# Optimization experiments

Hardware: AMD Instinct MI355X
Metric: run time of the kernel (lower is better)

Reference implementation:

```python
import jax, jax.numpy as jnp
import numpy as np

N, F, H, L = 1536, 32, 64, 3  # num_nodes, num_features, hidden, num_layers
NEG_SLOPE = 0.01
BN_EPS = 1e-5


def _lrelu(x):
    return jnp.where(x >= 0, x, NEG_SLOPE * x)


def _gin_layer(x, src, tgt, eps, w1, b1, w2, b2, g, be):
    # scatter-add aggregation: out[tgt] += x[src] (source_to_target flow)
    agg = jax.ops.segment_sum(x[src], tgt, num_segments=N)
    h = (1.0 + eps) * x + agg
    h = jax.nn.relu(h @ w1 + b1)
    h = jax.nn.relu(h @ w2 + b2)
    # BatchNorm1d, training-mode (batch statistics, biased variance)
    mean = jnp.mean(h, axis=0)
    var = jnp.mean((h - mean) ** 2, axis=0)
    return (h - mean) * jax.lax.rsqrt(var + BN_EPS) * g + be


def setup_inputs() -> dict:
    key = jax.random.key(0)
    ks = iter(jax.random.split(key, 40))

    def rn(shape, scale=0.05):
        return jax.random.normal(next(ks), shape, dtype=jnp.float32) * scale

    inp = {
        "x": rn((N, F), 1.0),
        "node_features": rn((N, F), 1.0),
        # conv1: F -> H
        "c1_eps": jnp.zeros((), jnp.float32),
        "c1_w1": rn((F, H)), "c1_b1": jnp.zeros((H,), jnp.float32),
        "c1_w2": rn((H, H)), "c1_b2": jnp.zeros((H,), jnp.float32),
        "c1_g": jnp.ones((H,), jnp.float32), "c1_be": jnp.zeros((H,), jnp.float32),
        # L-1 additional GIN convs: H -> H (stacked)
        "cv_eps": jnp.zeros((L - 1,), jnp.float32),
        "cv_w1": rn((L - 1, H, H)), "cv_b1": jnp.zeros((L - 1, H), jnp.float32),
        "cv_w2": rn((L - 1, H, H)), "cv_b2": jnp.zeros((L - 1, H), jnp.float32),
        "cv_g": jnp.ones((L - 1, H), jnp.float32), "cv_be": jnp.zeros((L - 1, H), jnp.float32),
        # projection head
        "lin1_w": rn((H, H)), "lin1_b": jnp.zeros((H,), jnp.float32),
        "lin2_w": rn((H, F)), "lin2_b": jnp.zeros((F,), jnp.float32),
        # edge predictor: 2F -> H -> H -> H -> 1
        "ep_w1": rn((2 * F, H)), "ep_b1": jnp.zeros((H,), jnp.float32),
        "ep_w2": rn((H, H)), "ep_b2": jnp.zeros((H,), jnp.float32),
        "ep_w3": rn((H, H)), "ep_b3": jnp.zeros((H,), jnp.float32),
        "ep_w4": rn((H, 1)), "ep_b4": jnp.zeros((1,), jnp.float32),
    }
    return inp


def reference(x, node_features, c1_eps, c1_w1, c1_b1, c1_w2, c1_b2, c1_g, c1_be,
              cv_eps, cv_w1, cv_b1, cv_w2, cv_b2, cv_g, cv_be,
              lin1_w, lin1_b, lin2_w, lin2_b,
              ep_w1, ep_b1, ep_w2, ep_b2, ep_w3, ep_b3, ep_w4, ep_b4):
    # complete-graph upper-triangular edge list (matches torch.combinations order)
    src, tgt = jnp.triu_indices(N, k=1)
    h = node_features  # forward ignores input x
    xinit = h
    h = _lrelu(_gin_layer(h, src, tgt, c1_eps, c1_w1, c1_b1, c1_w2, c1_b2, c1_g, c1_be))
    for i in range(L - 1):
        h = _lrelu(_gin_layer(h, src, tgt, cv_eps[i], cv_w1[i], cv_b1[i],
                              cv_w2[i], cv_b2[i], cv_g[i], cv_be[i]))
    h = _lrelu(h @ lin1_w + lin1_b)
    h = _lrelu(h @ lin2_w + lin2_b)
    h = h + xinit  # [N, F]

    # edge predictor: gather -> MLP -> sigmoid over E edges
    ef = jnp.concatenate([h[src], h[tgt]], axis=-1)  # [E, 2F]
    e = jax.nn.relu(ef @ ep_w1 + ep_b1)
    e = jax.nn.relu(e @ ep_w2 + ep_b2)
    e = jax.nn.relu(e @ ep_w3 + ep_b3)
    e = jax.nn.sigmoid(e @ ep_w4 + ep_b4)[:, 0]  # [E]

    probs = jnp.zeros((N, N), dtype=h.dtype)
    probs = probs.at[src, tgt].set(e).at[tgt, src].set(e)
    return probs
```

## Files before the change

### kernel.cpp

```cpp
#include <hip/hip_runtime.h>
#include <math.h>

#define NN 1536
#define FF 32
#define HH 64
#define EE (NN*(NN-1)/2)
#define EBLK 2493
#define BN_EPS 1e-5f
#define SLOPE 0.01f

typedef _Float16 v8h  __attribute__((ext_vector_type(8)));
typedef __fp16   v2hf __attribute__((ext_vector_type(2)));
typedef float    f32x4 __attribute__((ext_vector_type(4)));

union V8H { v8h v; v2hf h2[4]; float4 f4; };

__device__ __forceinline__ float lrelu_f(float v){ return v >= 0.f ? v : SLOPE*v; }
__device__ __forceinline__ f32x4 lrelu4(f32x4 v) {
  f32x4 r;
#pragma unroll
  for (int j = 0; j < 4; ++j) r[j] = v[j] >= 0.f ? v[j] : SLOPE*v[j];
  return r;
}

template<int DIN, bool FIRST>
__global__ __launch_bounds__(512) void k_gin(
    const float* __restrict__ zin,
    const float* __restrict__ gg, const float* __restrict__ be,
    const float* __restrict__ eps_p,
    const float* __restrict__ W1, const float* __restrict__ b1,
    const float* __restrict__ W2, const float* __restrict__ b2,
    float* __restrict__ zout,
    const float* __restrict__ pw2, const float* __restrict__ pw3,
    _Float16* __restrict__ pwf) {
  int bid = blockIdx.x, tid = threadIdx.x;
  if (FIRST && bid >= 96) {
    int i = (bid - 96)*512 + tid;
    if (i < 8192) {
      int mat = i >> 12, r = i & 4095;
      int k = r >> 6, cout = r & 63;
      int m = cout >> 4, cc = cout & 15;
      int q, g, b;
      if (mat == 0) { q = k >> 5; g = (k >> 3) & 3; b = k & 7; }
      else { int mF = k >> 4; g = (k >> 2) & 3; int rr = k & 3; q = mF >> 1; b = ((mF & 1) << 2) | rr; }
      const float* W = mat ? pw3 : pw2;
      pwf[mat*4096 + ((q*4 + m)*64 + (g*16 + cc))*8 + b] = (_Float16)W[r];
    }
    return;
  }

  __shared__ float W1s[DIN*64];
  __shared__ float W2s[4096];
  __shared__ float red[2048];
  __shared__ float redq[2048];
  __shared__ float scl[64], sft[64], pf[64];
  __shared__ float hh[16][64];
  __shared__ float uls[16*64];
  __shared__ float t1s[16][64];

  int c = tid & 63, y = tid >> 6;
  for (int i = tid; i < DIN*64; i += 512) W1s[i] = W1[i];
  for (int i = tid; i < 4096; i += 512)   W2s[i] = W2[i];

  constexpr int C4 = DIN/4;
  constexpr int RS = 512/C4;
  int col4 = tid % C4, rseg = tid / C4;
  const f32x4* z4 = (const f32x4*)zin;
  int r0 = bid*16;

  if (!FIRST) {
    f32x4 s0 = {0.f,0.f,0.f,0.f}, s1 = s0, s2 = s0, s3 = s0;
    f32x4 q0 = s0, q1 = s0, q2 = s0, q3 = s0;
    for (int n = rseg; n < NN; n += 4*RS) {
      f32x4 v0 = z4[n*C4 + col4];
      f32x4 v1 = z4[(n + RS)*C4 + col4];
      f32x4 v2 = z4[(n + 2*RS)*C4 + col4];
      f32x4 v3 = z4[(n + 3*RS)*C4 + col4];
      s0 += v0; q0 += v0*v0;
      s1 += v1; q1 += v1*v1;
      s2 += v2; q2 += v2*v2;
      s3 += v3; q3 += v3*v3;
    }
    f32x4 s4 = (s0 + s1) + (s2 + s3);
    f32x4 q4 = (q0 + q1) + (q2 + q3);
#pragma unroll
    for (int j = 0; j < 4; ++j) {
      red[rseg*DIN + col4*4 + j]  = s4[j];
      redq[rseg*DIN + col4*4 + j] = q4[j];
    }
    __syncthreads();
    if (tid < DIN) {
      float S = 0.f, Q = 0.f;
      for (int r = 0; r < RS; ++r) { S += red[r*DIN + tid]; Q += redq[r*DIN + tid]; }
      float m  = S * (1.f/NN);
      float iv = rsqrtf(Q * (1.f/NN) - m*m + BN_EPS);
      float sc = iv * gg[tid];
      scl[tid] = sc;
      sft[tid] = be[tid] - m*sc;
    }
    __syncthreads();
  }

  {
    f32x4 p0 = {0.f,0.f,0.f,0.f}, p1 = p0, p2 = p0, p3 = p0;
    f32x4 sc4, sh4;
    if (!FIRST) {
#pragma unroll
      for (int j = 0; j < 4; ++j) { sc4[j] = scl[col4*4 + j]; sh4[j] = sft[col4*4 + j]; }
    }
    int n = rseg;
    for (; n + 3*RS < r0; n += 4*RS) {
      f32x4 va = z4[n*C4 + col4];
      f32x4 vb = z4[(n + RS)*C4 + col4];
      f32x4 vc = z4[(n + 2*RS)*C4 + col4];
      f32x4 vd = z4[(n + 3*RS)*C4 + col4];
      if (!FIRST) {
        va = lrelu4(va*sc4 + sh4); vb = lrelu4(vb*sc4 + sh4);
        vc = lrelu4(vc*sc4 + sh4); vd = lrelu4(vd*sc4 + sh4);
      }
      p0 += va; p1 += vb; p2 += vc; p3 += vd;
    }
    for (; n < r0; n += RS) {
      f32x4 va = z4[n*C4 + col4];
      if (!FIRST) va = lrelu4(va*sc4 + sh4);
      p0 += va;
    }
    p0 = (p0 + p1) + (p2 + p3);
#pragma unroll
    for (int j = 0; j < 4; ++j) red[rseg*DIN + col4*4 + j] = p0[j];
    __syncthreads();
    if (tid < DIN) {
      float S = 0.f;
      for (int r = 0; r < RS; ++r) S += red[r*DIN + tid];
      pf[tid] = S;
    }
    __syncthreads();
  }

  float e1 = 1.f + eps_p[0];
  if (c < DIN) {
    for (int rr = y; rr < 16; rr += 8) {
      float v = zin[(r0 + rr)*DIN + c];
      hh[rr][c] = FIRST ? v : lrelu_f(v*scl[c] + sft[c]);
    }
  }
  __syncthreads();
  if (c < DIN) {
    for (int rr = y; rr < 16; rr += 8) {
      float run = pf[c];
      for (int r2 = 0; r2 < rr; ++r2) run += hh[r2][c];
      uls[rr*DIN + c] = e1*hh[rr][c] + run;
    }
  }
  __syncthreads();

  {
    float a0 = b1[c], a1 = a0;
    for (int k = 0; k < DIN; ++k) {
      float w = W1s[k*64 + c];
      a0 = fmaf(uls[y*DIN + k],       w, a0);
      a1 = fmaf(uls[(y + 8)*DIN + k], w, a1);
    }
    t1s[y][c]     = fmaxf(a0, 0.f);
    t1s[y + 8][c] = fmaxf(a1, 0.f);
  }
  __syncthreads();

  {
    float z0 = b2[c], z1 = z0;
    for (int k = 0; k < 64; ++k) {
      float w = W2s[k*64 + c];
      z0 = fmaf(t1s[y][k],     w, z0);
      z1 = fmaf(t1s[y + 8][k], w, z1);
    }
    zout[(r0 + y)*64 + c]     = fmaxf(z0, 0.f);
    zout[(r0 + y + 8)*64 + c] = fmaxf(z1, 0.f);
  }
}

__global__ __launch_bounds__(512) void k_head(
    const float* __restrict__ z,
    const float* __restrict__ gg, const float* __restrict__ be,
    const float* __restrict__ l1w, const float* __restrict__ l1b,
    const float* __restrict__ l2w, const float* __restrict__ l2b,
    const float* __restrict__ nf,
    const float* __restrict__ epw1, const float* __restrict__ epb1,
    _Float16* __restrict__ Ah, _Float16* __restrict__ Bh) {
  __shared__ float W1s[4096];
  __shared__ float W2s[2048];
  __shared__ float Was[2048];
  __shared__ float Wbs[2048];
  __shared__ float scratch[4096];
  __shared__ float scl[64], sft[64];
  int tid = threadIdx.x, c = tid & 63, y = tid >> 6;
  for (int i = tid; i < 4096; i += 512) W1s[i] = l1w[i];
  for (int i = tid; i < 2048; i += 512) { W2s[i] = l2w[i]; Was[i] = epw1[i]; Wbs[i] = epw1[2048 + i]; }

  {
    int col4 = tid & 15, rseg = tid >> 4;
    const f32x4* z4 = (const f32x4*)z;
    f32x4 s0 = {0.f,0.f,0.f,0.f}, s1 = s0, s2 = s0, s3 = s0;
    f32x4 q0 = s0, q1 = s0, q2 = s0, q3 = s0;
    for (int n = rseg; n < NN; n += 128) {
      f32x4 v0 = z4[n*16 + col4];
      f32x4 v1 = z4[(n + 32)*16 + col4];
      f32x4 v2 = z4[(n + 64)*16 + col4];
      f32x4 v3 = z4[(n + 96)*16 + col4];
      s0 += v0; q0 += v0*v0;
      s1 += v1; q1 += v1*v1;
      s2 += v2; q2 += v2*v2;
      s3 += v3; q3 += v3*v3;
    }
    f32x4 s4 = (s0 + s1) + (s2 + s3);
    f32x4 q4 = (q0 + q1) + (q2 + q3);
    float* red  = scratch;
    float* redq = scratch + 2048;
#pragma unroll
    for (int j = 0; j < 4; ++j) {
      red[rseg*64 + col4*4 + j]  = s4[j];
      redq[rseg*64 + col4*4 + j] = q4[j];
    }
    __syncthreads();
    if (tid < 64) {
      float S = 0.f, Q = 0.f;
      for (int r = 0; r < 32; ++r) { S += red[r*64 + tid]; Q += redq[r*64 + tid]; }
      float m  = S * (1.f/NN);
      float iv = rsqrtf(Q * (1.f/NN) - m*m + BN_EPS);
      float sc = iv * gg[tid];
      scl[tid] = sc;
      sft[tid] = be[tid] - m*sc;
    }
    __syncthreads();
  }

  float* t0 = scratch;
  float* t1 = scratch + 1024;
  float* t2 = scratch + 2048;
  int r0 = blockIdx.x*16;

  for (int rr = y; rr < 16; rr += 8)
    t0[rr*64 + c] = lrelu_f(z[(r0 + rr)*64 + c]*scl[c] + sft[c]);
  __syncthreads();
  {
    float a0 = l1b[c], a1 = a0;
    for (int k = 0; k < 64; ++k) {
      float w = W1s[k*64 + c];
      a0 = fmaf(t0[y*64 + k],       w, a0);
      a1 = fmaf(t0[(y + 8)*64 + k], w, a1);
    }
    t1[y*64 + c]       = lrelu_f(a0);
    t1[(y + 8)*64 + c] = lrelu_f(a1);
  }
  __syncthreads();
  if (c < 32) {
    float v0 = l2b[c], v1 = v0;
    for (int k = 0; k < 64; ++k) {
      float w = W2s[k*32 + c];
      v0 = fmaf(t1[y*64 + k],       w, v0);
      v1 = fmaf(t1[(y + 8)*64 + k], w, v1);
    }
    t2[y*32 + c]       = lrelu_f(v0) + nf[(r0 + y)*32 + c];
    t2[(y + 8)*32 + c] = lrelu_f(v1) + nf[(r0 + y + 8)*32 + c];
  }
  __syncthreads();
  {
    float av0 = epb1[c], av1 = av0;
    float bv0 = 0.f, bv1 = 0.f;
    for (int k = 0; k < 32; ++k) {
      float wa = Was[k*64 + c], wb = Wbs[k*64 + c];
      av0 = fmaf(t2[y*32 + k], wa, av0);       bv0 = fmaf(t2[y*32 + k], wb, bv0);
      av1 = fmaf(t2[(y + 8)*32 + k], wa, av1); bv1 = fmaf(t2[(y + 8)*32 + k], wb, bv1);
    }
    Ah[(r0 + y)*64 + c]     = (_Float16)av0;  Bh[(r0 + y)*64 + c]     = (_Float16)bv0;
    Ah[(r0 + y + 8)*64 + c] = (_Float16)av1;  Bh[(r0 + y + 8)*64 + c] = (_Float16)bv1;
  }
}

__global__ __launch_bounds__(256, 4) void k_edges_f16(
    const _Float16* __restrict__ Ah, const _Float16* __restrict__ Bh,
    const _Float16* __restrict__ Wf,
    const float* __restrict__ b2, const float* __restrict__ b3,
    const float* __restrict__ w4, const float* __restrict__ b4,
    float* __restrict__ out) {
  __shared__ _Float16 Wl[8192];
  int tid = threadIdx.x, wid = tid >> 6, lane = tid & 63;
  int c = lane & 15, g = lane >> 4;

  {
    const float4* src = (const float4*)Wf;
    float4* dst = (float4*)Wl;
    for (int i = tid; i < 1024; i += 256) dst[i] = src[i];
  }

  int w = blockIdx.x*4 + wid;
  int cum, kk, sbase;
  if (w < 1524) { cum = 0; kk = 12; sbase = 0; }
  else {
    cum = 1524; kk = 11; sbase = 127;
    while (kk > 1 && w >= cum + 128*kk) { cum += 128*kk; sbase += 128; --kk; }
  }
  int idx = w - cum;
  int q = idx / kk;
  int s = sbase + q;
  int t0 = s + 1 + ((idx - q*kk) << 7);

  f32x4 b2v[4], b3v[4];
  v2hf w4h[8];
  int g4 = g*4;
#pragma unroll
  for (int m = 0; m < 4; ++m) {
#pragma unroll
    for (int r = 0; r < 4; ++r) {
      int f = 16*m + g4 + r;
      b2v[m][r] = b2[f]; b3v[m][r] = b3[f];
    }
    v2hf wa = { (__fp16)w4[16*m + g4],     (__fp16)w4[16*m + g4 + 1] };
    v2hf wb = { (__fp16)w4[16*m + g4 + 2], (__fp16)w4[16*m + g4 + 3] };
    w4h[2*m] = wa; w4h[2*m + 1] = wb;
  }
  float b4v = b4[0];

  V8H zu; zu.f4 = make_float4(0.f, 0.f, 0.f, 0.f);
  const v8h vzero = zu.v;
  const v2hf z2 = { (__fp16)0.f, (__fp16)0.f };

  V8H a0, a1;
  a0.f4 = *(const float4*)(Ah + s*64 + g*8);
  a1.f4 = *(const float4*)(Ah + s*64 + 32 + g*8);

  int tl = t0 + c;
  V8H y0, y1;
  y0.f4 = *(const float4*)(Bh + tl*64 + g*8);
  y1.f4 = *(const float4*)(Bh + tl*64 + 32 + g*8);

  const v8h* wl = (const v8h*)Wl;
  __syncthreads();

  for (int it = 0; it < 8; ++it) {
    int tb = t0 + (it << 4);
    if (tb >= NN) break;
    int t = tb + c;

    V8H f0, f1;
    f0.v = __builtin_elementwise_max(a0.v + y0.v, vzero);
    f1.v = __builtin_elementwise_max(a1.v + y1.v, vzero);

    int tn = tb + 16 + c;
    y0.f4 = *(const float4*)(Bh + tn*64 + g*8);
    y1.f4 = *(const float4*)(Bh + tn*64 + 32 + g*8);

    __builtin_amdgcn_s_setprio(1);
    f32x4 acc[4];
#pragma unroll
    for (int m = 0; m < 4; ++m)
      acc[m] = __builtin_amdgcn_mfma_f32_16x16x32_f16(wl[m*64 + lane], f0.v, b2v[m], 0, 0, 0);
#pragma unroll
    for (int m = 0; m < 4; ++m)
      acc[m] = __builtin_amdgcn_mfma_f32_16x16x32_f16(wl[(4 + m)*64 + lane], f1.v, acc[m], 0, 0, 0);
    __builtin_amdgcn_s_setprio(0);

    V8H p0, p1;
#pragma unroll
    for (int m = 0; m < 2; ++m) {
      p0.h2[2*m]     = __builtin_elementwise_max(__builtin_amdgcn_cvt_pkrtz(acc[m][0],   acc[m][1]),   z2);
      p0.h2[2*m + 1] = __builtin_elementwise_max(__builtin_amdgcn_cvt_pkrtz(acc[m][2],   acc[m][3]),   z2);
      p1.h2[2*m]     = __builtin_elementwise_max(__builtin_amdgcn_cvt_pkrtz(acc[m+2][0], acc[m+2][1]), z2);
      p1.h2[2*m + 1] = __builtin_elementwise_max(__builtin_amdgcn_cvt_pkrtz(acc[m+2][2], acc[m+2][3]), z2);
    }

    __builtin_amdgcn_s_setprio(1);
    f32x4 acc3[4];
#pragma unroll
    for (int m = 0; m < 4; ++m)
      acc3[m] = __builtin_amdgcn_mfma_f32_16x16x32_f16(wl[512 + m*64 + lane], p0.v, b3v[m], 0, 0, 0);
#pragma unroll
    for (int m = 0; m < 4; ++m)
      acc3[m] = __builtin_amdgcn_mfma_f32_16x16x32_f16(wl[512 + (4 + m)*64 + lane], p1.v, acc3[m], 0, 0, 0);
    __builtin_amdgcn_s_setprio(0);

    float p = 0.f;
#pragma unroll
    for (int m = 0; m < 4; ++m) {
      v2hf l0 = __builtin_elementwise_max(
          __builtin_amdgcn_cvt_pkrtz(acc3[m][0], acc3[m][1]), z2);
      v2hf l1 = __builtin_elementwise_max(
          __builtin_amdgcn_cvt_pkrtz(acc3[m][2], acc3[m][3]), z2);
      p = __builtin_amdgcn_fdot2(l0, w4h[2*m],     p, false);
      p = __builtin_amdgcn_fdot2(l1, w4h[2*m + 1], p, false);
    }
    p += __shfl_xor(p, 16, 64);
    p += __shfl_xor(p, 32, 64);
    float ez = __builtin_amdgcn_exp2f(-1.44269504f * (p + b4v));
    float prob = __builtin_amdgcn_rcpf(1.f + ez);
    if (lane < 16 && t < NN) out[s*NN + t] = prob;
  }
}

__global__ __launch_bounds__(256) void k_mirror(float* __restrict__ out) {
  __shared__ float tile[32][33];
  int k = blockIdx.x;
  int bi = (int)((sqrtf(8.f*k + 1.f) - 1.f)*0.5f);
  while (bi*(bi + 1)/2 > k) --bi;
  while ((bi + 1)*(bi + 2)/2 <= k) ++bi;
  int bj = k - bi*(bi + 1)/2;
  int i0 = bi*32, j0 = bj*32;
  int tx = threadIdx.x & 31, ty = threadIdx.x >> 5;
#pragma unroll
  for (int r = 0; r < 4; ++r)
    tile[ty + r*8][tx] = out[(j0 + ty + r*8)*NN + i0 + tx];
  __syncthreads();
#pragma unroll
  for (int r = 0; r < 4; ++r) {
    int row = ty + r*8;
    int i = i0 + row, j = j0 + tx;
    if (bi > bj)      out[i*NN + j] = tile[tx][row];
    else if (i > j)   out[i*NN + j] = tile[tx][row];
    else if (i == j)  out[i*NN + j] = 0.f;
  }
}

extern "C" void kernel_launch(void* const* d_in, const int* in_sizes, int n_in,
                              void* d_out, int out_size, void* d_ws, size_t ws_size,
                              hipStream_t stream) {
  const float* nf     = (const float*)d_in[1];
  const float* c1_eps = (const float*)d_in[2];
  const float* c1_w1  = (const float*)d_in[3];
  const float* c1_b1  = (const float*)d_in[4];
  const float* c1_w2  = (const float*)d_in[5];
  const float* c1_b2  = (const float*)d_in[6];
  const float* c1_g   = (const float*)d_in[7];
  const float* c1_be  = (const float*)d_in[8];
  const float* cv_eps = (const float*)d_in[9];
  const float* cv_w1  = (const float*)d_in[10];
  const float* cv_b1  = (const float*)d_in[11];
  const float* cv_w2  = (const float*)d_in[12];
  const float* cv_b2  = (const float*)d_in[13];
  const float* cv_g   = (const float*)d_in[14];
  const float* cv_be  = (const float*)d_in[15];
  const float* lin1_w = (const float*)d_in[16];
  const float* lin1_b = (const float*)d_in[17];
  const float* lin2_w = (const float*)d_in[18];
  const float* lin2_b = (const float*)d_in[19];
  const float* ep_w1  = (const float*)d_in[20];
  const float* ep_b1  = (const float*)d_in[21];
  const float* ep_w2  = (const float*)d_in[22];
  const float* ep_b2  = (const float*)d_in[23];
  const float* ep_w3  = (const float*)d_in[24];
  const float* ep_b3  = (const float*)d_in[25];
  const float* ep_w4  = (const float*)d_in[26];
  const float* ep_b4  = (const float*)d_in[27];

  float* ws = (float*)d_ws;
  float* zA    = ws;
  float* zB    = zA + NN*64;
  _Float16* Ah = (_Float16*)(zB + NN*64);
  _Float16* Bh = Ah + NN*64;
  _Float16* Wf = Bh + NN*64;

  float* out = (float*)d_out;

  k_gin<32, true><<<112, 512, 0, stream>>>(nf, nullptr, nullptr, c1_eps,
      c1_w1, c1_b1, c1_w2, c1_b2, zA, ep_w2, ep_w3, Wf);

  k_gin<64, false><<<96, 512, 0, stream>>>(zA, c1_g, c1_be, cv_eps,
      cv_w1, cv_b1, cv_w2, cv_b2, zB, nullptr, nullptr, nullptr);

  k_gin<64, false><<<96, 512, 0, stream>>>(zB, cv_g, cv_be, cv_eps + 1,
      cv_w1 + HH*HH, cv_b1 + HH, cv_w2 + HH*HH, cv_b2 + HH, zA,
      nullptr, nullptr, nullptr);

  k_head<<<96, 512, 0, stream>>>(zA, cv_g + HH, cv_be + HH,
                                 lin1_w, lin1_b, lin2_w, lin2_b, nf,
                                 ep_w1, ep_b1, Ah, Bh);

  k_edges_f16<<<EBLK, 256, 0, stream>>>(Ah, Bh, Wf, ep_b2, ep_b3, ep_w4, ep_b4, out);

  k_mirror<<<1176, 256, 0, stream>>>(out);
}
```

Baseline: 87.04 us.

## Replace redundant per-block full scans with per-block partial sums and BN kernels

Before, each GIN block rescanned all N rows to compute the BatchNorm statistics and its prefix sum of earlier rows. Now each matmul block emits per-block column sums and sums of squares, and a small k_bn kernel builds the normalized activations plus per-block row sums. Each GIN block then forms its prefix from those 96 block sums. This removes O(N) redundant global reads per block, at the cost of two extra kernel launches and extra intermediate buffers.

```diff
diff --git a/kernel.cpp b/kernel.cpp
--- a/kernel.cpp
+++ b/kernel.cpp
@@ -16,26 +16,15 @@
 union V8H { v8h v; v2hf h2[4]; float4 f4; };
 
 __device__ __forceinline__ float lrelu_f(float v){ return v >= 0.f ? v : SLOPE*v; }
-__device__ __forceinline__ f32x4 lrelu4(f32x4 v) {
-  f32x4 r;
-#pragma unroll
-  for (int j = 0; j < 4; ++j) r[j] = v[j] >= 0.f ? v[j] : SLOPE*v[j];
-  return r;
-}
-
-template<int DIN, bool FIRST>
-__global__ __launch_bounds__(512) void k_gin(
-    const float* __restrict__ zin,
-    const float* __restrict__ gg, const float* __restrict__ be,
-    const float* __restrict__ eps_p,
-    const float* __restrict__ W1, const float* __restrict__ b1,
-    const float* __restrict__ W2, const float* __restrict__ b2,
-    float* __restrict__ zout,
+
+
+__global__ __launch_bounds__(256) void k_first(
+    const float* __restrict__ nf, float* __restrict__ H,
     const float* __restrict__ pw2, const float* __restrict__ pw3,
     _Float16* __restrict__ pwf) {
   int bid = blockIdx.x, tid = threadIdx.x;
-  if (FIRST && bid >= 96) {
-    int i = (bid - 96)*512 + tid;
+  if (bid >= 96) {
+    int i = (bid - 96)*256 + tid;
     if (i < 8192) {
       int mat = i >> 12, r = i & 4095;
       int k = r >> 6, cout = r & 63;
@@ -48,103 +37,100 @@
     }
     return;
   }
-
+  __shared__ float part[8][32];
+  int c = tid & 31, y = tid >> 5;
+  float s = nf[(bid*16 + y)*32 + c] + nf[(bid*16 + y + 8)*32 + c];
+  part[y][c] = s;
+  __syncthreads();
+  if (y == 0) {
+    float S = 0.f;
+#pragma unroll
+    for (int r = 0; r < 8; ++r) S += part[r][c];
+    H[bid*64 + c] = S;
+  }
+}
+
+__global__ __launch_bounds__(256) void k_bn(
+    const float* __restrict__ z, const float* __restrict__ P,
+    const float* __restrict__ gg, const float* __restrict__ be,
+    float* __restrict__ hbuf, float* __restrict__ H) {
+  __shared__ float sums[2][128];
+  __shared__ float scl[64], sft[64];
+  __shared__ float part[4][64];
+  int tid = threadIdx.x, bid = blockIdx.x;
+  {
+    int c2 = tid & 127, half = tid >> 7;
+    float S0 = 0.f, S1 = 0.f;
+    int j0 = half*48;
+    for (int j = j0; j < j0 + 48; j += 2) { S0 += P[j*128 + c2]; S1 += P[(j+1)*128 + c2]; }
+    sums[half][c2] = S0 + S1;
+  }
+  __syncthreads();
+  if (tid < 64) {
+    float S = sums[0][tid] + sums[1][tid];
+    float Q = sums[0][64 + tid] + sums[1][64 + tid];
+    float m  = S * (1.f/NN);
+    float iv = rsqrtf(Q * (1.f/NN) - m*m + BN_EPS);
+    float sc = iv * gg[tid];
+    scl[tid] = sc;
+    sft[tid] = be[tid] - m*sc;
+  }
+  __syncthreads();
+  int c = tid & 63, y = tid >> 6;
+  float sc = scl[c], sh = sft[c];
+  float hs = 0.f;
+#pragma unroll
+  for (int i = 0; i < 4; ++i) {
+    int rr = y + 4*i;
+    float h = lrelu_f(z[(bid*16 + rr)*64 + c]*sc + sh);
+    hbuf[(bid*16 + rr)*64 + c] = h;
+    hs += h;
+  }
+  part[y][c] = hs;
+  __syncthreads();
+  if (y == 0)
+    H[bid*64 + c] = part[0][c] + part[1][c] + part[2][c] + part[3][c];
+}
+
+template<int DIN>
+__global__ __launch_bounds__(512) void k_mmp(
+    const float* __restrict__ hb, const float* __restrict__ H,
+    const float* __restrict__ eps_p,
+    const float* __restrict__ W1, const float* __restrict__ b1,
+    const float* __restrict__ W2, const float* __restrict__ b2,
+    float* __restrict__ zout, float* __restrict__ P) {
   __shared__ float W1s[DIN*64];
   __shared__ float W2s[4096];
-  __shared__ float red[2048];
-  __shared__ float redq[2048];
-  __shared__ float scl[64], sft[64], pf[64];
-  __shared__ float hh[16][64];
-  __shared__ float uls[16*64];
+  __shared__ float red[8][64];
+  __shared__ float pf[64];
+  __shared__ float hh[16][DIN];
+  __shared__ float uls[16*DIN];
   __shared__ float t1s[16][64];
-
+  __shared__ float pp[8][64], pq[8][64];
+  int tid = threadIdx.x, bid = blockIdx.x;
   int c = tid & 63, y = tid >> 6;
   for (int i = tid; i < DIN*64; i += 512) W1s[i] = W1[i];
   for (int i = tid; i < 4096; i += 512)   W2s[i] = W2[i];
 
-  constexpr int C4 = DIN/4;
-  constexpr int RS = 512/C4;
-  int col4 = tid % C4, rseg = tid / C4;
-  const f32x4* z4 = (const f32x4*)zin;
-  int r0 = bid*16;
-
-  if (!FIRST) {
-    f32x4 s0 = {0.f,0.f,0.f,0.f}, s1 = s0, s2 = s0, s3 = s0;
-    f32x4 q0 = s0, q1 = s0, q2 = s0, q3 = s0;
-    for (int n = rseg; n < NN; n += 4*RS) {
-      f32x4 v0 = z4[n*C4 + col4];
-      f32x4 v1 = z4[(n + RS)*C4 + col4];
-      f32x4 v2 = z4[(n + 2*RS)*C4 + col4];
-      f32x4 v3 = z4[(n + 3*RS)*C4 + col4];
-      s0 += v0; q0 += v0*v0;
-      s1 += v1; q1 += v1*v1;
-      s2 += v2; q2 += v2*v2;
-      s3 += v3; q3 += v3*v3;
-    }
-    f32x4 s4 = (s0 + s1) + (s2 + s3);
-    f32x4 q4 = (q0 + q1) + (q2 + q3);
-#pragma unroll
-    for (int j = 0; j < 4; ++j) {
-      red[rseg*DIN + col4*4 + j]  = s4[j];
-      redq[rseg*DIN + col4*4 + j] = q4[j];
-    }
-    __syncthreads();
-    if (tid < DIN) {
-      float S = 0.f, Q = 0.f;
-      for (int r = 0; r < RS; ++r) { S += red[r*DIN + tid]; Q += redq[r*DIN + tid]; }
-      float m  = S * (1.f/NN);
-      float iv = rsqrtf(Q * (1.f/NN) - m*m + BN_EPS);
-      float sc = iv * gg[tid];
-      scl[tid] = sc;
-      sft[tid] = be[tid] - m*sc;
-    }
-    __syncthreads();
-  }
-
-  {
-    f32x4 p0 = {0.f,0.f,0.f,0.f}, p1 = p0, p2 = p0, p3 = p0;
-    f32x4 sc4, sh4;
-    if (!FIRST) {
-#pragma unroll
-      for (int j = 0; j < 4; ++j) { sc4[j] = scl[col4*4 + j]; sh4[j] = sft[col4*4 + j]; }
-    }
-    int n = rseg;
-    for (; n + 3*RS < r0; n += 4*RS) {
-      f32x4 va = z4[n*C4 + col4];
-      f32x4 vb = z4[(n + RS)*C4 + col4];
-      f32x4 vc = z4[(n + 2*RS)*C4 + col4];
-      f32x4 vd = z4[(n + 3*RS)*C4 + col4];
-      if (!FIRST) {
-        va = lrelu4(va*sc4 + sh4); vb = lrelu4(vb*sc4 + sh4);
-        vc = lrelu4(vc*sc4 + sh4); vd = lrelu4(vd*sc4 + sh4);
-      }
-      p0 += va; p1 += vb; p2 += vc; p3 += vd;
-    }
-    for (; n < r0; n += RS) {
-      f32x4 va = z4[n*C4 + col4];
-      if (!FIRST) va = lrelu4(va*sc4 + sh4);
-      p0 += va;
-    }
-    p0 = (p0 + p1) + (p2 + p3);
-#pragma unroll
-    for (int j = 0; j < 4; ++j) red[rseg*DIN + col4*4 + j] = p0[j];
-    __syncthreads();
-    if (tid < DIN) {
-      float S = 0.f;
-      for (int r = 0; r < RS; ++r) S += red[r*DIN + tid];
-      pf[tid] = S;
-    }
-    __syncthreads();
-  }
+  {
+    float s = 0.f;
+    if (c < DIN) for (int j = y; j < bid; j += 8) s += H[j*64 + c];
+    red[y][c] = s;
+  }
+  if (c < DIN) {
+    hh[y][c]     = hb[(bid*16 + y)*DIN + c];
+    hh[y + 8][c] = hb[(bid*16 + y + 8)*DIN + c];
+  }
+  __syncthreads();
+  if (y == 0 && c < DIN) {
+    float S = 0.f;
+#pragma unroll
+    for (int r = 0; r < 8; ++r) S += red[r][c];
+    pf[c] = S;
+  }
+  __syncthreads();
 
   float e1 = 1.f + eps_p[0];
-  if (c < DIN) {
-    for (int rr = y; rr < 16; rr += 8) {
-      float v = zin[(r0 + rr)*DIN + c];
-      hh[rr][c] = FIRST ? v : lrelu_f(v*scl[c] + sft[c]);
-    }
-  }
-  __syncthreads();
   if (c < DIN) {
     for (int rr = y; rr < 16; rr += 8) {
       float run = pf[c];
@@ -154,32 +140,40 @@
   }
   __syncthreads();
 
-  {
-    float a0 = b1[c], a1 = a0;
-    for (int k = 0; k < DIN; ++k) {
-      float w = W1s[k*64 + c];
-      a0 = fmaf(uls[y*DIN + k],       w, a0);
-      a1 = fmaf(uls[(y + 8)*DIN + k], w, a1);
-    }
-    t1s[y][c]     = fmaxf(a0, 0.f);
-    t1s[y + 8][c] = fmaxf(a1, 0.f);
-  }
-  __syncthreads();
-
-  {
-    float z0 = b2[c], z1 = z0;
-    for (int k = 0; k < 64; ++k) {
-      float w = W2s[k*64 + c];
-      z0 = fmaf(t1s[y][k],     w, z0);
-      z1 = fmaf(t1s[y + 8][k], w, z1);
-    }
-    zout[(r0 + y)*64 + c]     = fmaxf(z0, 0.f);
-    zout[(r0 + y + 8)*64 + c] = fmaxf(z1, 0.f);
-  }
-}
-
-__global__ __launch_bounds__(512) void k_head(
-    const float* __restrict__ z,
+  float a0 = b1[c], a1 = a0;
+  for (int k = 0; k < DIN; ++k) {
+    float w = W1s[k*64 + c];
+    a0 = fmaf(uls[y*DIN + k],       w, a0);
+    a1 = fmaf(uls[(y + 8)*DIN + k], w, a1);
+  }
+  t1s[y][c]     = fmaxf(a0, 0.f);
+  t1s[y + 8][c] = fmaxf(a1, 0.f);
+  __syncthreads();
+
+  float z0 = b2[c], z1 = z0;
+  for (int k = 0; k < 64; ++k) {
+    float w = W2s[k*64 + c];
+    z0 = fmaf(t1s[y][k],     w, z0);
+    z1 = fmaf(t1s[y + 8][k], w, z1);
+  }
+  z0 = fmaxf(z0, 0.f); z1 = fmaxf(z1, 0.f);
+  zout[(bid*16 + y)*64 + c]     = z0;
+  zout[(bid*16 + y + 8)*64 + c] = z1;
+
+  pp[y][c] = z0 + z1;
+  pq[y][c] = z0*z0 + z1*z1;
+  __syncthreads();
+  if (y == 0) {
+    float S = 0.f, Q = 0.f;
+#pragma unroll
+    for (int r = 0; r < 8; ++r) { S += pp[r][c]; Q += pq[r][c]; }
+    P[bid*128 + c]      = S;
+    P[bid*128 + 64 + c] = Q;
+  }
+}
+
+__global__ __launch_bounds__(512) void k_head2(
+    const float* __restrict__ z, const float* __restrict__ P,
     const float* __restrict__ gg, const float* __restrict__ be,
     const float* __restrict__ l1w, const float* __restrict__ l1b,
     const float* __restrict__ l2w, const float* __restrict__ l2b,
@@ -190,6 +184,7 @@
   __shared__ float W2s[2048];
   __shared__ float Was[2048];
   __shared__ float Wbs[2048];
+  __shared__ float sums[4][128];
   __shared__ float scratch[4096];
   __shared__ float scl[64], sft[64];
   int tid = threadIdx.x, c = tid & 63, y = tid >> 6;
@@ -197,41 +192,22 @@
   for (int i = tid; i < 2048; i += 512) { W2s[i] = l2w[i]; Was[i] = epw1[i]; Wbs[i] = epw1[2048 + i]; }
 
   {
-    int col4 = tid & 15, rseg = tid >> 4;
-    const f32x4* z4 = (const f32x4*)z;
-    f32x4 s0 = {0.f,0.f,0.f,0.f}, s1 = s0, s2 = s0, s3 = s0;
-    f32x4 q0 = s0, q1 = s0, q2 = s0, q3 = s0;
-    for (int n = rseg; n < NN; n += 128) {
-      f32x4 v0 = z4[n*16 + col4];
-      f32x4 v1 = z4[(n + 32)*16 + col4];
-      f32x4 v2 = z4[(n + 64)*16 + col4];
-      f32x4 v3 = z4[(n + 96)*16 + col4];
-      s0 += v0; q0 += v0*v0;
-      s1 += v1; q1 += v1*v1;
-      s2 += v2; q2 += v2*v2;
-      s3 += v3; q3 += v3*v3;
-    }
-    f32x4 s4 = (s0 + s1) + (s2 + s3);
-    f32x4 q4 = (q0 + q1) + (q2 + q3);
-    float* red  = scratch;
-    float* redq = scratch + 2048;
-#pragma unroll
-    for (int j = 0; j < 4; ++j) {
-      red[rseg*64 + col4*4 + j]  = s4[j];
-      redq[rseg*64 + col4*4 + j] = q4[j];
-    }
-    __syncthreads();
-    if (tid < 64) {
-      float S = 0.f, Q = 0.f;
-      for (int r = 0; r < 32; ++r) { S += red[r*64 + tid]; Q += redq[r*64 + tid]; }
-      float m  = S * (1.f/NN);
-      float iv = rsqrtf(Q * (1.f/NN) - m*m + BN_EPS);
-      float sc = iv * gg[tid];
-      scl[tid] = sc;
-      sft[tid] = be[tid] - m*sc;
-    }
-    __syncthreads();
-  }
+    int c2 = tid & 127, q = tid >> 7;
+    float S = 0.f;
+    for (int j = q*24; j < q*24 + 24; ++j) S += P[j*128 + c2];
+    sums[q][c2] = S;
+  }
+  __syncthreads();
+  if (tid < 64) {
+    float S = sums[0][tid] + sums[1][tid] + sums[2][tid] + sums[3][tid];
+    float Q = sums[0][64+tid] + sums[1][64+tid] + sums[2][64+tid] + sums[3][64+tid];
+    float m  = S * (1.f/NN);
+    float iv = rsqrtf(Q * (1.f/NN) - m*m + BN_EPS);
+    float sc = iv * gg[tid];
+    scl[tid] = sc;
+    sft[tid] = be[tid] - m*sc;
+  }
+  __syncthreads();
 
   float* t0 = scratch;
   float* t1 = scratch + 1024;
@@ -453,27 +429,29 @@
   float* ws = (float*)d_ws;
   float* zA    = ws;
   float* zB    = zA + NN*64;
-  _Float16* Ah = (_Float16*)(zB + NN*64);
+  float* hbuf  = zB + NN*64;
+  float* H     = hbuf + NN*64;
+  float* P     = H + 96*64;
+  _Float16* Ah = (_Float16*)(P + 96*128);
   _Float16* Bh = Ah + NN*64;
   _Float16* Wf = Bh + NN*64;
 
   float* out = (float*)d_out;
 
-  k_gin<32, true><<<112, 512, 0, stream>>>(nf, nullptr, nullptr, c1_eps,
-      c1_w1, c1_b1, c1_w2, c1_b2, zA, ep_w2, ep_w3, Wf);
-
-  k_gin<64, false><<<96, 512, 0, stream>>>(zA, c1_g, c1_be, cv_eps,
-      cv_w1, cv_b1, cv_w2, cv_b2, zB, nullptr, nullptr, nullptr);
-
-  k_gin<64, false><<<96, 512, 0, stream>>>(zB, cv_g, cv_be, cv_eps + 1,
-      cv_w1 + HH*HH, cv_b1 + HH, cv_w2 + HH*HH, cv_b2 + HH, zA,
-      nullptr, nullptr, nullptr);
-
-  k_head<<<96, 512, 0, stream>>>(zA, cv_g + HH, cv_be + HH,
-                                 lin1_w, lin1_b, lin2_w, lin2_b, nf,
-                                 ep_w1, ep_b1, Ah, Bh);
+  k_first<<<128, 256, 0, stream>>>(nf, H, ep_w2, ep_w3, Wf);
+  k_mmp<32><<<96, 512, 0, stream>>>(nf, H, c1_eps, c1_w1, c1_b1, c1_w2, c1_b2, zA, P);
+
+  k_bn<<<96, 256, 0, stream>>>(zA, P, c1_g, c1_be, hbuf, H);
+  k_mmp<64><<<96, 512, 0, stream>>>(hbuf, H, cv_eps, cv_w1, cv_b1, cv_w2, cv_b2, zB, P);
+
+  k_bn<<<96, 256, 0, stream>>>(zB, P, cv_g, cv_be, hbuf, H);
+  k_mmp<64><<<96, 512, 0, stream>>>(hbuf, H, cv_eps + 1,
+      cv_w1 + HH*HH, cv_b1 + HH, cv_w2 + HH*HH, cv_b2 + HH, zA, P);
+
+  k_head2<<<96, 512, 0, stream>>>(zA, P, cv_g + HH, cv_be + HH,
+                                  lin1_w, lin1_b, lin2_w, lin2_b, nf,
+                                  ep_w1, ep_b1, Ah, Bh);
 
   k_edges_f16<<<EBLK, 256, 0, stream>>>(Ah, Bh, Wf, ep_b2, ep_b3, ep_w4, ep_b4, out);
-
   k_mirror<<<1176, 256, 0, stream>>>(out);
 }
```

Result: faster. 81.20 us (-6.7%).
